# Kernel tuning notes

Measured on AMD Instinct MI355X. Metric: run time of the kernel, lower is better.

The kernel has to match this reference:

```python
import jax, jax.numpy as jnp
import numpy as np

N_NODES = 50000
N_EDGES = 400000
IN_DIM, HID_DIM, OUT_DIM = 512, 512, 128


def sage_conv(x, src, dst, W_l, b_l, W_r, n_nodes):
    # PyG SAGEConv (mean aggr): out = lin_l(mean_{j in N(i)} x_j) + lin_r(x_i)
    msgs = x[src]                                             # [E, d_in]
    agg = jax.ops.segment_sum(msgs, dst, num_segments=n_nodes)
    deg = jax.ops.segment_sum(jnp.ones((src.shape[0],), x.dtype), dst,
                              num_segments=n_nodes)
    mean = agg / jnp.maximum(deg, 1.0)[:, None]
    return mean @ W_l + b_l + x @ W_r


def setup_inputs() -> dict:
    key = jax.random.key(0)
    ks = jax.random.split(key, 9)
    x = jax.random.normal(ks[0], (N_NODES, IN_DIM), dtype=jnp.float32)
    edge_index = jax.random.randint(ks[1], (2, N_EDGES), 0, N_NODES, dtype=jnp.int32)

    def glorot(k, d_in, d_out):
        s = (6.0 / (d_in + d_out)) ** 0.5
        return jax.random.uniform(k, (d_in, d_out), jnp.float32, -s, s)

    return {
        "x": x,
        "edge_index": edge_index,
        "W1_l": glorot(ks[2], IN_DIM, HID_DIM),
        "b1": jnp.zeros((HID_DIM,), jnp.float32),
        "W1_r": glorot(ks[3], IN_DIM, HID_DIM),
        "W2_l": glorot(ks[4], HID_DIM, HID_DIM),
        "b2": jnp.zeros((HID_DIM,), jnp.float32),
        "W2_r": glorot(ks[5], HID_DIM, HID_DIM),
        "W3_l": glorot(ks[6], HID_DIM, OUT_DIM),
        "b3": jnp.zeros((OUT_DIM,), jnp.float32),
        "W3_r": glorot(ks[7], HID_DIM, OUT_DIM),
    }


def reference(x, edge_index, W1_l, b1, W1_r, W2_l, b2, W2_r, W3_l, b3, W3_r):
    src, dst = edge_index[0], edge_index[1]
    n = x.shape[0]
    h = sage_conv(x, src, dst, W1_l, b1, W1_r, n)
    h = jax.nn.relu(h)  # dropout is identity in eval mode
    h = sage_conv(h, src, dst, W2_l, b2, W2_r, n)
    h = jax.nn.relu(h)
    h = sage_conv(h, src, dst, W3_l, b3, W3_r, n)
    return jax.nn.log_softmax(h, axis=-1)
```

## Files before the change

kernel.cpp:

```cpp
#include <hip/hip_runtime.h>
#include <hip/hip_bf16.h>


#define N_NODES 50000
#define N_EDGES 400000

typedef unsigned short u16;
typedef unsigned int u32;
typedef __attribute__((ext_vector_type(8))) short short8;
typedef __attribute__((ext_vector_type(4))) float floatx4;

__device__ __forceinline__ u16 f32_to_bf16(float f) {
    u32 u = __float_as_uint(f);
    u32 r = 0x7FFFu + ((u >> 16) & 1u);
    return (u16)((u + r) >> 16);
}
__device__ __forceinline__ float bf16_to_f32(u32 lo16) {
    return __uint_as_float(lo16 << 16);
}

__global__ __launch_bounds__(256) void zero4_kernel(float4* __restrict__ p, int n4) {
    int i = blockIdx.x * 256 + threadIdx.x;
    if (i < n4) p[i] = make_float4(0.f, 0.f, 0.f, 0.f);
}

__global__ __launch_bounds__(256) void hist_kernel(const int* __restrict__ dst,
                                                   int* __restrict__ deg, int E) {
    int e = blockIdx.x * 256 + threadIdx.x;
    if (e < E) atomicAdd(&deg[dst[e]], 1);
}

__global__ __launch_bounds__(256) void scan_reduce(const int* __restrict__ v,
                                                   int* __restrict__ bsums, int n) {
    __shared__ int sh[256];
    int i = blockIdx.x * 256 + threadIdx.x;
    sh[threadIdx.x] = (i < n) ? v[i] : 0;
    __syncthreads();
    for (int off = 128; off > 0; off >>= 1) {
        if (threadIdx.x < off) sh[threadIdx.x] += sh[threadIdx.x + off];
        __syncthreads();
    }
    if (threadIdx.x == 0) bsums[blockIdx.x] = sh[0];
}

__global__ __launch_bounds__(256) void scan_sums(int* __restrict__ bsums, int nb) {
    __shared__ int sh[256];
    int t = threadIdx.x;
    int val = (t < nb) ? bsums[t] : 0;
    sh[t] = val;
    __syncthreads();
    for (int off = 1; off < 256; off <<= 1) {
        int v = (t >= off) ? sh[t - off] : 0;
        __syncthreads();
        sh[t] += v;
        __syncthreads();
    }
    if (t < nb) bsums[t] = sh[t] - val;
}

__global__ __launch_bounds__(256) void scan_final(int* __restrict__ v,
                                                  const int* __restrict__ bsums, int n) {
    __shared__ int sh[256];
    int t = threadIdx.x;
    int i = blockIdx.x * 256 + t;
    int val = (i < n) ? v[i] : 0;
    sh[t] = val;
    __syncthreads();
    for (int off = 1; off < 256; off <<= 1) {
        int x = (t >= off) ? sh[t - off] : 0;
        __syncthreads();
        sh[t] += x;
        __syncthreads();
    }
    int excl = sh[t] - val + bsums[blockIdx.x];
    if (i < n) v[i] = excl;
    if (i == n - 1) v[n] = excl + val;
}

__global__ __launch_bounds__(256) void fill_kernel(const int* __restrict__ src,
                                                   const int* __restrict__ dst,
                                                   const int* __restrict__ row_start,
                                                   int* __restrict__ cursor,
                                                   int* __restrict__ csr_src, int E) {
    int e = blockIdx.x * 256 + threadIdx.x;
    if (e < E) {
        int d = dst[e];
        int pos = row_start[d] + atomicAdd(&cursor[d], 1);
        csr_src[pos] = src[e];
    }
}

__global__ __launch_bounds__(256) void convert_bf16(const float* __restrict__ in,
                                                    u16* __restrict__ out, int n8) {
    int i = blockIdx.x * 256 + threadIdx.x;
    if (i >= n8) return;
    const float4* p = (const float4*)in + (size_t)i * 2;
    float4 v0 = p[0], v1 = p[1];
    uint4 o;
    o.x = (u32)f32_to_bf16(v0.x) | ((u32)f32_to_bf16(v0.y) << 16);
    o.y = (u32)f32_to_bf16(v0.z) | ((u32)f32_to_bf16(v0.w) << 16);
    o.z = (u32)f32_to_bf16(v1.x) | ((u32)f32_to_bf16(v1.y) << 16);
    o.w = (u32)f32_to_bf16(v1.z) | ((u32)f32_to_bf16(v1.w) << 16);
    ((uint4*)out)[i] = o;
}

__global__ __launch_bounds__(256) void transpose_w(const float* __restrict__ W,
                                                   u16* __restrict__ WT,
                                                   int K, int N) {
    __shared__ float t[32][33];
    int n0 = blockIdx.x * 32, k0 = blockIdx.y * 32;
    int c = threadIdx.x & 31, r0 = threadIdx.x >> 5;
    for (int r = r0; r < 32; r += 8)
        t[r][c] = W[(size_t)(k0 + r) * N + n0 + c];
    __syncthreads();
    for (int r = r0; r < 32; r += 8)
        WT[(size_t)(n0 + r) * K + k0 + c] = f32_to_bf16(t[c][r]);
}

__global__ __launch_bounds__(256) void gather_mean_bf16(const u16* __restrict__ X,
                                                        const int* __restrict__ row_start,
                                                        const int* __restrict__ csr_src,
                                                        u16* __restrict__ agg, int M) {
    int node = (blockIdx.x * 256 + threadIdx.x) >> 6;
    int lane = threadIdx.x & 63;
    if (node >= M) return;
    int beg = row_start[node], end = row_start[node + 1];
    float a[8] = {0.f, 0.f, 0.f, 0.f, 0.f, 0.f, 0.f, 0.f};
    for (int c = beg; c < end; c += 64) {
        int nb = min(64, end - c);
        int eid = (lane < nb) ? csr_src[c + lane] : 0;
        for (int i = 0; i < nb; ++i) {
            int s = __shfl(eid, i);
            uint4 v = ((const uint4*)(X + (size_t)s * 512))[lane];
            a[0] += bf16_to_f32(v.x & 0xffffu); a[1] += bf16_to_f32(v.x >> 16);
            a[2] += bf16_to_f32(v.y & 0xffffu); a[3] += bf16_to_f32(v.y >> 16);
            a[4] += bf16_to_f32(v.z & 0xffffu); a[5] += bf16_to_f32(v.z >> 16);
            a[6] += bf16_to_f32(v.w & 0xffffu); a[7] += bf16_to_f32(v.w >> 16);
        }
    }
    float inv = 1.0f / fmaxf((float)(end - beg), 1.0f);
    uint4 o;
    o.x = (u32)f32_to_bf16(a[0] * inv) | ((u32)f32_to_bf16(a[1] * inv) << 16);
    o.y = (u32)f32_to_bf16(a[2] * inv) | ((u32)f32_to_bf16(a[3] * inv) << 16);
    o.z = (u32)f32_to_bf16(a[4] * inv) | ((u32)f32_to_bf16(a[5] * inv) << 16);
    o.w = (u32)f32_to_bf16(a[6] * inv) | ((u32)f32_to_bf16(a[7] * inv) << 16);
    ((uint4*)(agg + (size_t)node * 512))[lane] = o;
}

#define LDSROW 40

__global__ __launch_bounds__(256) void gemm_bf16(
    const u16* __restrict__ A1, const u16* __restrict__ A2,
    const u16* __restrict__ B1T, const u16* __restrict__ B2T,
    const float* __restrict__ bias,
    u16* __restrict__ Cb, float* __restrict__ Cf,
    int M, int N, int relu, int nStrips, int nCols) {
    __shared__ u16 As[2][128 * LDSROW];
    __shared__ u16 Bs[2][128 * LDSROW];

    int strip, colt;
    if (nCols == 4) {
        int b = blockIdx.x;
        int g = b >> 5, w5 = b & 31;
        strip = g * 8 + (w5 & 7);
        colt = w5 >> 3;
        if (strip >= nStrips) return;
    } else {
        strip = blockIdx.x;
        colt = 0;
    }
    const int row0 = strip * 128, col0 = colt * 128;

    const int t = threadIdx.x;
    const int w = t >> 6, lane = t & 63;
    const int wm = (w >> 1) * 64, wn = (w & 1) * 64;
    const int l15 = lane & 15, kq = lane >> 4;

    floatx4 acc[4][4];
#pragma unroll
    for (int i = 0; i < 4; ++i)
#pragma unroll
        for (int j = 0; j < 4; ++j) acc[i][j] = floatx4{0.f, 0.f, 0.f, 0.f};

    const int sr = t >> 2;
    const int sce = (t & 3) * 8;
    const size_t aoffS0 = (size_t)min(row0 + sr, M - 1) * 512 + sce;
    const size_t aoffS1 = (size_t)min(row0 + 64 + sr, M - 1) * 512 + sce;
    const size_t boffS0 = (size_t)(col0 + sr) * 512 + sce;
    const size_t boffS1 = (size_t)(col0 + 64 + sr) * 512 + sce;
    const int ldsS0 = sr * LDSROW + sce;
    const int ldsS1 = (sr + 64) * LDSROW + sce;

    uint4 ra0, ra1, rb0, rb1;
    auto loadTile = [&](int it) {
        int k0 = it * 32;
        const u16* Ap = (k0 < 512) ? A1 : A2;
        const u16* Bp = (k0 < 512) ? B1T : B2T;
        int eff = k0 & 511;
        ra0 = *(const uint4*)(Ap + aoffS0 + eff);
        ra1 = *(const uint4*)(Ap + aoffS1 + eff);
        rb0 = *(const uint4*)(Bp + boffS0 + eff);
        rb1 = *(const uint4*)(Bp + boffS1 + eff);
    };

    loadTile(0);
    for (int it = 0; it < 32; ++it) {
        const int buf = it & 1;
        *(uint4*)&As[buf][ldsS0] = ra0;
        *(uint4*)&As[buf][ldsS1] = ra1;
        *(uint4*)&Bs[buf][ldsS0] = rb0;
        *(uint4*)&Bs[buf][ldsS1] = rb1;
        __syncthreads();
        if (it + 1 < 32) loadTile(it + 1);

        short8 a[4], b[4];
#pragma unroll
        for (int mt = 0; mt < 4; ++mt)
            a[mt] = *(const short8*)&As[buf][(wm + mt * 16 + l15) * LDSROW + kq * 8];
#pragma unroll
        for (int nt = 0; nt < 4; ++nt)
            b[nt] = *(const short8*)&Bs[buf][(wn + nt * 16 + l15) * LDSROW + kq * 8];
#pragma unroll
        for (int mt = 0; mt < 4; ++mt)
#pragma unroll
            for (int nt = 0; nt < 4; ++nt)
                acc[mt][nt] = __builtin_amdgcn_mfma_f32_16x16x32_bf16(
                    b[nt], a[mt], acc[mt][nt], 0, 0, 0);
    }

#pragma unroll
    for (int mt = 0; mt < 4; ++mt) {
        int row = row0 + wm + mt * 16 + l15;
        if (row >= M) continue;
#pragma unroll
        for (int nt = 0; nt < 4; ++nt) {
            int c0 = col0 + wn + nt * 16 + kq * 4;
            float4 bb = *(const float4*)(bias + c0);
            float v0 = acc[mt][nt][0] + bb.x;
            float v1 = acc[mt][nt][1] + bb.y;
            float v2 = acc[mt][nt][2] + bb.z;
            float v3 = acc[mt][nt][3] + bb.w;
            if (relu) {
                v0 = fmaxf(v0, 0.f); v1 = fmaxf(v1, 0.f);
                v2 = fmaxf(v2, 0.f); v3 = fmaxf(v3, 0.f);
            }
            if (Cf) {
                *(float4*)(Cf + (size_t)row * N + c0) = make_float4(v0, v1, v2, v3);
            } else {
                uint2 o;
                o.x = (u32)f32_to_bf16(v0) | ((u32)f32_to_bf16(v1) << 16);
                o.y = (u32)f32_to_bf16(v2) | ((u32)f32_to_bf16(v3) << 16);
                *(uint2*)(Cb + (size_t)row * N + c0) = o;
            }
        }
    }
}

__global__ __launch_bounds__(256) void logsoftmax128(float* __restrict__ out, int M) {
    int row = blockIdx.x * 4 + (threadIdx.x >> 6);
    int lane = threadIdx.x & 63;
    if (row >= M) return;
    float* p = out + (size_t)row * 128;
    float a = p[lane];
    float b = p[lane + 64];
    float m = fmaxf(a, b);
#pragma unroll
    for (int off = 32; off > 0; off >>= 1) m = fmaxf(m, __shfl_xor(m, off));
    float s = expf(a - m) + expf(b - m);
#pragma unroll
    for (int off = 32; off > 0; off >>= 1) s += __shfl_xor(s, off);
    float ls = m + logf(s);
    p[lane] = a - ls;
    p[lane + 64] = b - ls;
}

extern "C" void kernel_launch(void* const* d_in, const int* in_sizes, int n_in,
                              void* d_out, int out_size, void* d_ws, size_t ws_size,
                              hipStream_t stream) {
    const float* x    = (const float*)d_in[0];
    const int*   ei   = (const int*)d_in[1];
    const float* W1_l = (const float*)d_in[2];
    const float* b1   = (const float*)d_in[3];
    const float* W1_r = (const float*)d_in[4];
    const float* W2_l = (const float*)d_in[5];
    const float* b2   = (const float*)d_in[6];
    const float* W2_r = (const float*)d_in[7];
    const float* W3_l = (const float*)d_in[8];
    const float* b3   = (const float*)d_in[9];
    const float* W3_r = (const float*)d_in[10];
    float* out = (float*)d_out;

    const int* src = ei;
    const int* dst = ei + N_EDGES;

    char* base = (char*)d_ws;
    int* row_start = (int*)(base);
    int* cursor    = (int*)(base + 200208);
    int* bsums     = (int*)(base + 400416);
    int* csr_src   = (int*)(base + 402464);
    u16* xb   = (u16*)(base + 2002464);
    u16* aggb = (u16*)(base + 53202464);
    u16* h1b  = (u16*)(base + 104402464);
    u16* h2b  = (u16*)(base + 155602464);
    u16* w1lT = (u16*)(base + 206802464);
    u16* w1rT = (u16*)(base + 207326752);
    u16* w2lT = (u16*)(base + 207851040);
    u16* w2rT = (u16*)(base + 208375328);
    u16* w3lT = (u16*)(base + 208899616);
    u16* w3rT = (u16*)(base + 209030688);

    const int E = N_EDGES, M = N_NODES;
    const int nblk = (M + 255) / 256;

    zero4_kernel<<<(25154 + 255) / 256, 256, 0, stream>>>((float4*)d_ws, 25154);
    hist_kernel<<<(E + 255) / 256, 256, 0, stream>>>(dst, row_start, E);
    scan_reduce<<<nblk, 256, 0, stream>>>(row_start, bsums, M);
    scan_sums<<<1, 256, 0, stream>>>(bsums, nblk);
    scan_final<<<nblk, 256, 0, stream>>>(row_start, bsums, M);
    fill_kernel<<<(E + 255) / 256, 256, 0, stream>>>(src, dst, row_start, cursor,
                                                     csr_src, E);

    convert_bf16<<<(3200000 + 255) / 256, 256, 0, stream>>>(x, xb, 3200000);
    transpose_w<<<dim3(16, 16), 256, 0, stream>>>(W1_l, w1lT, 512, 512);
    transpose_w<<<dim3(16, 16), 256, 0, stream>>>(W1_r, w1rT, 512, 512);
    transpose_w<<<dim3(16, 16), 256, 0, stream>>>(W2_l, w2lT, 512, 512);
    transpose_w<<<dim3(16, 16), 256, 0, stream>>>(W2_r, w2rT, 512, 512);
    transpose_w<<<dim3(4, 16), 256, 0, stream>>>(W3_l, w3lT, 512, 128);
    transpose_w<<<dim3(4, 16), 256, 0, stream>>>(W3_r, w3rT, 512, 128);

    const int gather_blocks = (M * 64 + 255) / 256;
    const int nStrips = (M + 127) / 128;
    const int bigGrid = ((nStrips + 7) / 8) * 32;

    gather_mean_bf16<<<gather_blocks, 256, 0, stream>>>(xb, row_start, csr_src, aggb, M);
    gemm_bf16<<<bigGrid, 256, 0, stream>>>(aggb, xb, w1lT, w1rT, b1,
                                           h1b, nullptr, M, 512, 1, nStrips, 4);
    gather_mean_bf16<<<gather_blocks, 256, 0, stream>>>(h1b, row_start, csr_src, aggb, M);
    gemm_bf16<<<bigGrid, 256, 0, stream>>>(aggb, h1b, w2lT, w2rT, b2,
                                           h2b, nullptr, M, 512, 1, nStrips, 4);
    gather_mean_bf16<<<gather_blocks, 256, 0, stream>>>(h2b, row_start, csr_src, aggb, M);
    gemm_bf16<<<nStrips, 256, 0, stream>>>(aggb, h2b, w3lT, w3rT, b3,
                                           nullptr, out, M, 128, 0, nStrips, 1);

    logsoftmax128<<<(M + 3) / 4, 256, 0, stream>>>(out, M);
}
```

Before: 709.9 us.

## Transform before aggregating: GEMM with concatenated weights, then gather-mean with fused epilogue

Reorders each SAGE layer so the node features are first multiplied by [W_l | W_r] in one GEMM over K=512, and the neighbor mean is then taken over the transformed rows. The gather fuses the bias, root term, ReLU and, in the last layer, log-softmax. The final layer therefore gathers 128-wide rows instead of 512-wide ones, and the separate aggregation buffer and logsoftmax pass are removed. It also switches the GEMM's LDS layout from padded rows to an XOR swizzle. The cost is an extra bf16 rounding of the transformed features before averaging and a larger Yl/Yr workspace.

```diff
diff --git a/kernel.cpp b/kernel.cpp
--- a/kernel.cpp
+++ b/kernel.cpp
@@ -117,10 +117,101 @@
         WT[(size_t)(n0 + r) * K + k0 + c] = f32_to_bf16(t[c][r]);
 }
 
-__global__ __launch_bounds__(256) void gather_mean_bf16(const u16* __restrict__ X,
-                                                        const int* __restrict__ row_start,
-                                                        const int* __restrict__ csr_src,
-                                                        u16* __restrict__ agg, int M) {
+__global__ __launch_bounds__(256) void gemm_bf16(
+    const u16* __restrict__ A, const u16* __restrict__ BT,
+    u16* __restrict__ Cl, u16* __restrict__ Cr,
+    int M, int split, int nStrips, int nCols) {
+    __shared__ u16 As[2][4096];
+    __shared__ u16 Bs[2][4096];
+
+    const int grp = 8 * nCols;
+    int b = blockIdx.x;
+    int strip = (b / grp) * 8 + (b & 7);
+    int colt = (b % grp) >> 3;
+    if (strip >= nStrips) return;
+    const int row0 = strip * 128, col0 = colt * 128;
+
+    const int t = threadIdx.x;
+    const int w = t >> 6, lane = t & 63;
+    const int wm = (w >> 1) * 64, wn = (w & 1) * 64;
+    const int l15 = lane & 15, kq = lane >> 4;
+    const int swz = (l15 >> 1) & 3;
+
+    floatx4 acc[4][4];
+#pragma unroll
+    for (int i = 0; i < 4; ++i)
+#pragma unroll
+        for (int j = 0; j < 4; ++j) acc[i][j] = floatx4{0.f, 0.f, 0.f, 0.f};
+
+    const int sr = t >> 2;
+    const int sc = t & 3;
+    const size_t aoffS0 = (size_t)min(row0 + sr, M - 1) * 512 + sc * 8;
+    const size_t aoffS1 = (size_t)min(row0 + 64 + sr, M - 1) * 512 + sc * 8;
+    const size_t boffS0 = (size_t)(col0 + sr) * 512 + sc * 8;
+    const size_t boffS1 = (size_t)(col0 + 64 + sr) * 512 + sc * 8;
+    const int swzS = (sr >> 1) & 3;
+    const int ldsS0 = sr * 32 + (sc ^ swzS) * 8;
+    const int ldsS1 = (sr + 64) * 32 + (sc ^ swzS) * 8;
+
+    uint4 ra0, ra1, rb0, rb1;
+    auto loadTile = [&](int it) {
+        int eff = it * 32;
+        ra0 = *(const uint4*)(A + aoffS0 + eff);
+        ra1 = *(const uint4*)(A + aoffS1 + eff);
+        rb0 = *(const uint4*)(BT + boffS0 + eff);
+        rb1 = *(const uint4*)(BT + boffS1 + eff);
+    };
+
+    loadTile(0);
+    for (int it = 0; it < 16; ++it) {
+        const int buf = it & 1;
+        *(uint4*)&As[buf][ldsS0] = ra0;
+        *(uint4*)&As[buf][ldsS1] = ra1;
+        *(uint4*)&Bs[buf][ldsS0] = rb0;
+        *(uint4*)&Bs[buf][ldsS1] = rb1;
+        __syncthreads();
+        if (it + 1 < 16) loadTile(it + 1);
+
+        const int kc = (kq ^ swz) * 8;
+        short8 a[4], b[4];
+#pragma unroll
+        for (int mt = 0; mt < 4; ++mt)
+            a[mt] = *(const short8*)&As[buf][(wm + mt * 16 + l15) * 32 + kc];
+#pragma unroll
+        for (int nt = 0; nt < 4; ++nt)
+            b[nt] = *(const short8*)&Bs[buf][(wn + nt * 16 + l15) * 32 + kc];
+#pragma unroll
+        for (int mt = 0; mt < 4; ++mt)
+#pragma unroll
+            for (int nt = 0; nt < 4; ++nt)
+                acc[mt][nt] = __builtin_amdgcn_mfma_f32_16x16x32_bf16(
+                    b[nt], a[mt], acc[mt][nt], 0, 0, 0);
+    }
+
+    u16* __restrict__ Cbase = (col0 < split) ? Cl : Cr;
+    const int cadj = (col0 < split) ? col0 : (col0 - split);
+#pragma unroll
+    for (int mt = 0; mt < 4; ++mt) {
+        int row = row0 + wm + mt * 16 + l15;
+        if (row >= M) continue;
+#pragma unroll
+        for (int nt = 0; nt < 4; ++nt) {
+            int c0 = cadj + wn + nt * 16 + kq * 4;
+            uint2 o;
+            o.x = (u32)f32_to_bf16(acc[mt][nt][0]) |
+                  ((u32)f32_to_bf16(acc[mt][nt][1]) << 16);
+            o.y = (u32)f32_to_bf16(acc[mt][nt][2]) |
+                  ((u32)f32_to_bf16(acc[mt][nt][3]) << 16);
+            *(uint2*)(Cbase + (size_t)row * split + c0) = o;
+        }
+    }
+}
+
+__global__ __launch_bounds__(256) void gather_add_relu512(
+    const u16* __restrict__ Yl, const u16* __restrict__ Yr,
+    const float* __restrict__ bias,
+    const int* __restrict__ row_start, const int* __restrict__ csr_src,
+    u16* __restrict__ h, int M) {
     int node = (blockIdx.x * 256 + threadIdx.x) >> 6;
     int lane = threadIdx.x & 63;
     if (node >= M) return;
@@ -131,7 +222,7 @@
         int eid = (lane < nb) ? csr_src[c + lane] : 0;
         for (int i = 0; i < nb; ++i) {
             int s = __shfl(eid, i);
-            uint4 v = ((const uint4*)(X + (size_t)s * 512))[lane];
+            uint4 v = ((const uint4*)(Yl + (size_t)s * 512))[lane];
             a[0] += bf16_to_f32(v.x & 0xffffu); a[1] += bf16_to_f32(v.x >> 16);
             a[2] += bf16_to_f32(v.y & 0xffffu); a[3] += bf16_to_f32(v.y >> 16);
             a[4] += bf16_to_f32(v.z & 0xffffu); a[5] += bf16_to_f32(v.z >> 16);
@@ -139,139 +230,76 @@
         }
     }
     float inv = 1.0f / fmaxf((float)(end - beg), 1.0f);
+    uint4 yr = ((const uint4*)(Yr + (size_t)node * 512))[lane];
+    float4 b0 = ((const float4*)bias)[lane * 2];
+    float4 b1 = ((const float4*)bias)[lane * 2 + 1];
+    float v0 = fmaxf(a[0] * inv + bf16_to_f32(yr.x & 0xffffu) + b0.x, 0.f);
+    float v1 = fmaxf(a[1] * inv + bf16_to_f32(yr.x >> 16)     + b0.y, 0.f);
+    float v2 = fmaxf(a[2] * inv + bf16_to_f32(yr.y & 0xffffu) + b0.z, 0.f);
+    float v3 = fmaxf(a[3] * inv + bf16_to_f32(yr.y >> 16)     + b0.w, 0.f);
+    float v4 = fmaxf(a[4] * inv + bf16_to_f32(yr.z & 0xffffu) + b1.x, 0.f);
+    float v5 = fmaxf(a[5] * inv + bf16_to_f32(yr.z >> 16)     + b1.y, 0.f);
+    float v6 = fmaxf(a[6] * inv + bf16_to_f32(yr.w & 0xffffu) + b1.z, 0.f);
+    float v7 = fmaxf(a[7] * inv + bf16_to_f32(yr.w >> 16)     + b1.w, 0.f);
     uint4 o;
-    o.x = (u32)f32_to_bf16(a[0] * inv) | ((u32)f32_to_bf16(a[1] * inv) << 16);
-    o.y = (u32)f32_to_bf16(a[2] * inv) | ((u32)f32_to_bf16(a[3] * inv) << 16);
-    o.z = (u32)f32_to_bf16(a[4] * inv) | ((u32)f32_to_bf16(a[5] * inv) << 16);
-    o.w = (u32)f32_to_bf16(a[6] * inv) | ((u32)f32_to_bf16(a[7] * inv) << 16);
-    ((uint4*)(agg + (size_t)node * 512))[lane] = o;
-}
-
-#define LDSROW 40
-
-__global__ __launch_bounds__(256) void gemm_bf16(
-    const u16* __restrict__ A1, const u16* __restrict__ A2,
-    const u16* __restrict__ B1T, const u16* __restrict__ B2T,
+    o.x = (u32)f32_to_bf16(v0) | ((u32)f32_to_bf16(v1) << 16);
+    o.y = (u32)f32_to_bf16(v2) | ((u32)f32_to_bf16(v3) << 16);
+    o.z = (u32)f32_to_bf16(v4) | ((u32)f32_to_bf16(v5) << 16);
+    o.w = (u32)f32_to_bf16(v6) | ((u32)f32_to_bf16(v7) << 16);
+    ((uint4*)(h + (size_t)node * 512))[lane] = o;
+}
+
+__global__ __launch_bounds__(256) void gather_add_lsm128(
+    const u16* __restrict__ Yl, const u16* __restrict__ Yr,
     const float* __restrict__ bias,
-    u16* __restrict__ Cb, float* __restrict__ Cf,
-    int M, int N, int relu, int nStrips, int nCols) {
-    __shared__ u16 As[2][128 * LDSROW];
-    __shared__ u16 Bs[2][128 * LDSROW];
-
-    int strip, colt;
-    if (nCols == 4) {
-        int b = blockIdx.x;
-        int g = b >> 5, w5 = b & 31;
-        strip = g * 8 + (w5 & 7);
-        colt = w5 >> 3;
-        if (strip >= nStrips) return;
-    } else {
-        strip = blockIdx.x;
-        colt = 0;
-    }
-    const int row0 = strip * 128, col0 = colt * 128;
-
-    const int t = threadIdx.x;
-    const int w = t >> 6, lane = t & 63;
-    const int wm = (w >> 1) * 64, wn = (w & 1) * 64;
-    const int l15 = lane & 15, kq = lane >> 4;
-
-    floatx4 acc[4][4];
-#pragma unroll
-    for (int i = 0; i < 4; ++i)
-#pragma unroll
-        for (int j = 0; j < 4; ++j) acc[i][j] = floatx4{0.f, 0.f, 0.f, 0.f};
-
-    const int sr = t >> 2;
-    const int sce = (t & 3) * 8;
-    const size_t aoffS0 = (size_t)min(row0 + sr, M - 1) * 512 + sce;
-    const size_t aoffS1 = (size_t)min(row0 + 64 + sr, M - 1) * 512 + sce;
-    const size_t boffS0 = (size_t)(col0 + sr) * 512 + sce;
-    const size_t boffS1 = (size_t)(col0 + 64 + sr) * 512 + sce;
-    const int ldsS0 = sr * LDSROW + sce;
-    const int ldsS1 = (sr + 64) * LDSROW + sce;
-
-    uint4 ra0, ra1, rb0, rb1;
-    auto loadTile = [&](int it) {
-        int k0 = it * 32;
-        const u16* Ap = (k0 < 512) ? A1 : A2;
-        const u16* Bp = (k0 < 512) ? B1T : B2T;
-        int eff = k0 & 511;
-        ra0 = *(const uint4*)(Ap + aoffS0 + eff);
-        ra1 = *(const uint4*)(Ap + aoffS1 + eff);
-        rb0 = *(const uint4*)(Bp + boffS0 + eff);
-        rb1 = *(const uint4*)(Bp + boffS1 + eff);
-    };
-
-    loadTile(0);
-    for (int it = 0; it < 32; ++it) {
-        const int buf = it & 1;
-        *(uint4*)&As[buf][ldsS0] = ra0;
-        *(uint4*)&As[buf][ldsS1] = ra1;
-        *(uint4*)&Bs[buf][ldsS0] = rb0;
-        *(uint4*)&Bs[buf][ldsS1] = rb1;
-        __syncthreads();
-        if (it + 1 < 32) loadTile(it + 1);
-
-        short8 a[4], b[4];
-#pragma unroll
-        for (int mt = 0; mt < 4; ++mt)
-            a[mt] = *(const short8*)&As[buf][(wm + mt * 16 + l15) * LDSROW + kq * 8];
-#pragma unroll
-        for (int nt = 0; nt < 4; ++nt)
-            b[nt] = *(const short8*)&Bs[buf][(wn + nt * 16 + l15) * LDSROW + kq * 8];
-#pragma unroll
-        for (int mt = 0; mt < 4; ++mt)
-#pragma unroll
-            for (int nt = 0; nt < 4; ++nt)
-                acc[mt][nt] = __builtin_amdgcn_mfma_f32_16x16x32_bf16(
-                    b[nt], a[mt], acc[mt][nt], 0, 0, 0);
-    }
-
-#pragma unroll
-    for (int mt = 0; mt < 4; ++mt) {
-        int row = row0 + wm + mt * 16 + l15;
-        if (row >= M) continue;
-#pragma unroll
-        for (int nt = 0; nt < 4; ++nt) {
-            int c0 = col0 + wn + nt * 16 + kq * 4;
-            float4 bb = *(const float4*)(bias + c0);
-            float v0 = acc[mt][nt][0] + bb.x;
-            float v1 = acc[mt][nt][1] + bb.y;
-            float v2 = acc[mt][nt][2] + bb.z;
-            float v3 = acc[mt][nt][3] + bb.w;
-            if (relu) {
-                v0 = fmaxf(v0, 0.f); v1 = fmaxf(v1, 0.f);
-                v2 = fmaxf(v2, 0.f); v3 = fmaxf(v3, 0.f);
-            }
-            if (Cf) {
-                *(float4*)(Cf + (size_t)row * N + c0) = make_float4(v0, v1, v2, v3);
-            } else {
-                uint2 o;
-                o.x = (u32)f32_to_bf16(v0) | ((u32)f32_to_bf16(v1) << 16);
-                o.y = (u32)f32_to_bf16(v2) | ((u32)f32_to_bf16(v3) << 16);
-                *(uint2*)(Cb + (size_t)row * N + c0) = o;
-            }
+    const int* __restrict__ row_start, const int* __restrict__ csr_src,
+    float* __restrict__ out, int M) {
+    int node = blockIdx.x * 16 + (threadIdx.x >> 4);
+    int lane = threadIdx.x & 63;
+    int li = lane & 15;
+    int gbase = lane & 48;
+    if (node >= M) return;
+    int beg = row_start[node], end = row_start[node + 1];
+    float a[8] = {0.f, 0.f, 0.f, 0.f, 0.f, 0.f, 0.f, 0.f};
+    for (int c = beg; c < end; c += 16) {
+        int nb = min(16, end - c);
+        int eid = (li < nb) ? csr_src[c + li] : 0;
+        for (int i = 0; i < nb; ++i) {
+            int s = __shfl(eid, gbase + i);
+            uint4 v = ((const uint4*)(Yl + (size_t)s * 128))[li];
+            a[0] += bf16_to_f32(v.x & 0xffffu); a[1] += bf16_to_f32(v.x >> 16);
+            a[2] += bf16_to_f32(v.y & 0xffffu); a[3] += bf16_to_f32(v.y >> 16);
+            a[4] += bf16_to_f32(v.z & 0xffffu); a[5] += bf16_to_f32(v.z >> 16);
+            a[6] += bf16_to_f32(v.w & 0xffffu); a[7] += bf16_to_f32(v.w >> 16);
         }
     }
-}
-
-__global__ __launch_bounds__(256) void logsoftmax128(float* __restrict__ out, int M) {
-    int row = blockIdx.x * 4 + (threadIdx.x >> 6);
-    int lane = threadIdx.x & 63;
-    if (row >= M) return;
-    float* p = out + (size_t)row * 128;
-    float a = p[lane];
-    float b = p[lane + 64];
-    float m = fmaxf(a, b);
-#pragma unroll
-    for (int off = 32; off > 0; off >>= 1) m = fmaxf(m, __shfl_xor(m, off));
-    float s = expf(a - m) + expf(b - m);
-#pragma unroll
-    for (int off = 32; off > 0; off >>= 1) s += __shfl_xor(s, off);
+    float inv = 1.0f / fmaxf((float)(end - beg), 1.0f);
+    uint4 yr = ((const uint4*)(Yr + (size_t)node * 128))[li];
+    float4 b0 = ((const float4*)bias)[li * 2];
+    float4 b1 = ((const float4*)bias)[li * 2 + 1];
+    float v[8];
+    v[0] = a[0] * inv + bf16_to_f32(yr.x & 0xffffu) + b0.x;
+    v[1] = a[1] * inv + bf16_to_f32(yr.x >> 16)     + b0.y;
+    v[2] = a[2] * inv + bf16_to_f32(yr.y & 0xffffu) + b0.z;
+    v[3] = a[3] * inv + bf16_to_f32(yr.y >> 16)     + b0.w;
+    v[4] = a[4] * inv + bf16_to_f32(yr.z & 0xffffu) + b1.x;
+    v[5] = a[5] * inv + bf16_to_f32(yr.z >> 16)     + b1.y;
+    v[6] = a[6] * inv + bf16_to_f32(yr.w & 0xffffu) + b1.z;
+    v[7] = a[7] * inv + bf16_to_f32(yr.w >> 16)     + b1.w;
+    float m = v[0];
+#pragma unroll
+    for (int j = 1; j < 8; ++j) m = fmaxf(m, v[j]);
+#pragma unroll
+    for (int off = 1; off < 16; off <<= 1) m = fmaxf(m, __shfl_xor(m, off));
+    float s = 0.f;
+#pragma unroll
+    for (int j = 0; j < 8; ++j) s += expf(v[j] - m);
+#pragma unroll
+    for (int off = 1; off < 16; off <<= 1) s += __shfl_xor(s, off);
     float ls = m + logf(s);
-    p[lane] = a - ls;
-    p[lane + 64] = b - ls;
+    float* p = out + (size_t)node * 128 + li * 8;
+    *(float4*)p       = make_float4(v[0] - ls, v[1] - ls, v[2] - ls, v[3] - ls);
+    *(float4*)(p + 4) = make_float4(v[4] - ls, v[5] - ls, v[6] - ls, v[7] - ls);
 }
 
 extern "C" void kernel_launch(void* const* d_in, const int* in_sizes, int n_in,
@@ -298,16 +326,14 @@
     int* cursor    = (int*)(base + 200208);
     int* bsums     = (int*)(base + 400416);
     int* csr_src   = (int*)(base + 402464);
-    u16* xb   = (u16*)(base + 2002464);
-    u16* aggb = (u16*)(base + 53202464);
-    u16* h1b  = (u16*)(base + 104402464);
-    u16* h2b  = (u16*)(base + 155602464);
-    u16* w1lT = (u16*)(base + 206802464);
-    u16* w1rT = (u16*)(base + 207326752);
-    u16* w2lT = (u16*)(base + 207851040);
-    u16* w2rT = (u16*)(base + 208375328);
-    u16* w3lT = (u16*)(base + 208899616);
-    u16* w3rT = (u16*)(base + 209030688);
+    u16* xb  = (u16*)(base + 2002464);
+    u16* h1b = (u16*)(base + 53202464);
+    u16* h2b = (u16*)(base + 104402464);
+    u16* Yl  = (u16*)(base + 155602464);
+    u16* Yr  = (u16*)(base + 206802464);
+    u16* w1T = (u16*)(base + 258002464);
+    u16* w2T = (u16*)(base + 259051040);
+    u16* w3T = (u16*)(base + 260099616);
 
     const int E = N_EDGES, M = N_NODES;
     const int nblk = (M + 255) / 256;
@@ -321,26 +347,26 @@
                                                      csr_src, E);
 
     convert_bf16<<<(3200000 + 255) / 256, 256, 0, stream>>>(x, xb, 3200000);
-    transpose_w<<<dim3(16, 16), 256, 0, stream>>>(W1_l, w1lT, 512, 512);
-    transpose_w<<<dim3(16, 16), 256, 0, stream>>>(W1_r, w1rT, 512, 512);
-    transpose_w<<<dim3(16, 16), 256, 0, stream>>>(W2_l, w2lT, 512, 512);
-    transpose_w<<<dim3(16, 16), 256, 0, stream>>>(W2_r, w2rT, 512, 512);
-    transpose_w<<<dim3(4, 16), 256, 0, stream>>>(W3_l, w3lT, 512, 128);
-    transpose_w<<<dim3(4, 16), 256, 0, stream>>>(W3_r, w3rT, 512, 128);
-
-    const int gather_blocks = (M * 64 + 255) / 256;
+    transpose_w<<<dim3(16, 16), 256, 0, stream>>>(W1_l, w1T, 512, 512);
+    transpose_w<<<dim3(16, 16), 256, 0, stream>>>(W1_r, w1T + 512 * 512, 512, 512);
+    transpose_w<<<dim3(16, 16), 256, 0, stream>>>(W2_l, w2T, 512, 512);
+    transpose_w<<<dim3(16, 16), 256, 0, stream>>>(W2_r, w2T + 512 * 512, 512, 512);
+    transpose_w<<<dim3(4, 16), 256, 0, stream>>>(W3_l, w3T, 512, 128);
+    transpose_w<<<dim3(4, 16), 256, 0, stream>>>(W3_r, w3T + 128 * 512, 512, 128);
+
     const int nStrips = (M + 127) / 128;
-    const int bigGrid = ((nStrips + 7) / 8) * 32;
-
-    gather_mean_bf16<<<gather_blocks, 256, 0, stream>>>(xb, row_start, csr_src, aggb, M);
-    gemm_bf16<<<bigGrid, 256, 0, stream>>>(aggb, xb, w1lT, w1rT, b1,
-                                           h1b, nullptr, M, 512, 1, nStrips, 4);
-    gather_mean_bf16<<<gather_blocks, 256, 0, stream>>>(h1b, row_start, csr_src, aggb, M);
-    gemm_bf16<<<bigGrid, 256, 0, stream>>>(aggb, h1b, w2lT, w2rT, b2,
-                                           h2b, nullptr, M, 512, 1, nStrips, 4);
-    gather_mean_bf16<<<gather_blocks, 256, 0, stream>>>(h2b, row_start, csr_src, aggb, M);
-    gemm_bf16<<<nStrips, 256, 0, stream>>>(aggb, h2b, w3lT, w3rT, b3,
-                                           nullptr, out, M, 128, 0, nStrips, 1);
-
-    logsoftmax128<<<(M + 3) / 4, 256, 0, stream>>>(out, M);
-}
+    const int grid8 = ((nStrips + 7) / 8) * 64;
+    const int grid2 = ((nStrips + 7) / 8) * 16;
+    const int gblocks = (M * 64 + 255) / 256;
+    const int g16blocks = (M + 15) / 16;
+
+    gemm_bf16<<<grid8, 256, 0, stream>>>(xb, w1T, Yl, Yr, M, 512, nStrips, 8);
+    gather_add_relu512<<<gblocks, 256, 0, stream>>>(Yl, Yr, b1, row_start,
+                                                    csr_src, h1b, M);
+    gemm_bf16<<<grid8, 256, 0, stream>>>(h1b, w2T, Yl, Yr, M, 512, nStrips, 8);
+    gather_add_relu512<<<gblocks, 256, 0, stream>>>(Yl, Yr, b2, row_start,
+                                                    csr_src, h2b, M);
+    gemm_bf16<<<grid2, 256, 0, stream>>>(h2b, w3T, Yl, Yr, M, 128, nStrips, 2);
+    gather_add_lsm128<<<g16blocks, 256, 0, stream>>>(Yl, Yr, b3, row_start,
+                                                     csr_src, out, M);
+}
```

Measured after the change: 660.1 us. 7.0% less time.
